# Performance work log

Measured on AMD Instinct MI355X. Metric: run time of the kernel, lower is better.

Reference implementation:

```python
import jax, jax.numpy as jnp
import numpy as np

IN_F = 4096
OUT_F = 11008
BATCH = 4
SEQ = 2048


def setup_inputs() -> dict:
    key = jax.random.key(0)
    kx, kw, ks = jax.random.split(key, 3)
    x = jax.random.normal(kx, (BATCH, SEQ, IN_F), dtype=jnp.float32)
    # simulated int4 weights stored in an int container, range [0, 16)
    W_q = jax.random.randint(kw, (OUT_F, IN_F), 0, 16, dtype=jnp.int32)
    scale = jax.random.uniform(ks, (OUT_F,), dtype=jnp.float32)
    return {"x": x, "W_q": W_q, "scale": scale}


def reference(x, W_q, scale):
    # dequantize: per-output-channel scale, then y = x @ W_fp^T
    W_fp = W_q.astype(jnp.float32) * scale[:, None]  # [out, in]
    return jnp.einsum('bsi,oi->bso', x, W_fp)
```

## Files before the change

kernel.cpp:

```cpp
#include <hip/hip_runtime.h>
#include <math.h>

#define M_DIM 8192
#define N_DIM 11008
#define K_DIM 4096

#define BM 256
#define BN 128
#define BKB 128
#define NT (K_DIM / BKB)
#define NBN (N_DIM / BN)
#define NWG ((M_DIM / BM) * NBN)

#define B_OFF 32768

typedef int int4v __attribute__((ext_vector_type(4)));
typedef int int16v __attribute__((ext_vector_type(16)));

__device__ __forceinline__ void async_copy16(const void* g, void* l) {
  __builtin_amdgcn_global_load_lds(
      (const __attribute__((address_space(1))) void*)g,
      (__attribute__((address_space(3))) void*)l, 16, 0, 0);
}

__global__ __launch_bounds__(256) void quant_x(const float* __restrict__ x,
                                               signed char* __restrict__ xq,
                                               float* __restrict__ sx) {
  __shared__ float wred[4];
  const int row = blockIdx.x;
  const int tid = threadIdx.x;
  const float4* src = (const float4*)(x + (size_t)row * K_DIM) + tid * 4;
  float4 v0 = src[0], v1 = src[1], v2 = src[2], v3 = src[3];

  float m = 0.f;
#define MX4(V) m = fmaxf(m, fmaxf(fmaxf(fabsf(V.x), fabsf(V.y)), fmaxf(fabsf(V.z), fabsf(V.w))))
  MX4(v0); MX4(v1); MX4(v2); MX4(v3);
#undef MX4
#pragma unroll
  for (int off = 32; off >= 1; off >>= 1)
    m = fmaxf(m, __shfl_xor(m, off, 64));
  if ((tid & 63) == 0) wred[tid >> 6] = m;
  __syncthreads();
  float smax = fmaxf(fmaxf(wred[0], wred[1]), fmaxf(wred[2], wred[3]));
  smax = fmaxf(smax, 1e-20f);
  const float inv = 127.f / smax;

  int4v o;
#define Q4(V, G) o[G] = ((int)rintf(V.x * inv) & 255) | (((int)rintf(V.y * inv) & 255) << 8) | \
                        (((int)rintf(V.z * inv) & 255) << 16) | (((int)rintf(V.w * inv) & 255) << 24)
  Q4(v0, 0); Q4(v1, 1); Q4(v2, 2); Q4(v3, 3);
#undef Q4
  ((int4v*)(xq + (size_t)row * K_DIM))[tid] = o;
  if (tid == 0) sx[row] = smax / 127.f;
}

__global__ __launch_bounds__(256) void pack_w(const int* __restrict__ in,
                                              signed char* __restrict__ wq) {
  const int idx = blockIdx.x * 256 + threadIdx.x;
  const int4* in4 = (const int4*)in + (size_t)idx * 4;
  int4 a = in4[0], b = in4[1], c = in4[2], d = in4[3];
  int4v o;
  o[0] = a.x | (a.y << 8) | (a.z << 16) | (a.w << 24);
  o[1] = b.x | (b.y << 8) | (b.z << 16) | (b.w << 24);
  o[2] = c.x | (c.y << 8) | (c.z << 16) | (c.w << 24);
  o[3] = d.x | (d.y << 8) | (d.z << 16) | (d.w << 24);
  ((int4v*)wq)[idx] = o;
}

__device__ __forceinline__ void stage_g(const signed char* __restrict__ P,
                                        int grow0, int k0b, char* dest, int tid) {
  const int r = tid >> 3;
  const int key = (r & 7) ^ ((tid >> 7) & 1);
  const int c = (tid & 7) ^ key;
  async_copy16(&P[(size_t)(grow0 + r) * K_DIM + k0b + c * 16], dest + tid * 16);
}

__global__ __launch_bounds__(512, 2) void gemm_i8(
    const signed char* __restrict__ A, const signed char* __restrict__ B,
    const float* __restrict__ scale, const float* __restrict__ sx,
    float* __restrict__ out) {
  __shared__ __align__(16) char smw[49152];
  const int tid = threadIdx.x;
  const int lane = tid & 63;
  const int wv = tid >> 6;
  const int wr = wv >> 1, wc = wv & 1;
  const int l31 = lane & 31;
  const int h = lane >> 5;
  const int swz = (l31 & 7) ^ ((l31 >> 4) & 1);

  int id = blockIdx.x;
  id = (id & 7) * (NWG / 8) + (id >> 3);
  const int bn = (id % NBN) * BN;
  const int bm = (id / NBN) * BM;

  int16v acc[2][2] = {};

#pragma unroll 1
  for (int t = 0; t < NT; ++t) {
    const int kb = t * BKB;
    __builtin_amdgcn_s_barrier();
    stage_g(A, bm,       kb, smw,         tid);
    stage_g(A, bm + 64,  kb, smw +  8192, tid);
    stage_g(A, bm + 128, kb, smw + 16384, tid);
    stage_g(A, bm + 192, kb, smw + 24576, tid);
    stage_g(B, bn,       kb, smw + B_OFF,        tid);
    stage_g(B, bn + 64,  kb, smw + B_OFF + 8192, tid);
    asm volatile("s_waitcnt vmcnt(0)" ::: "memory");
    __builtin_amdgcn_s_barrier();

#pragma unroll
    for (int ks = 0; ks < 4; ++ks) {
      const int cb = ((2 * ks + h) ^ swz) * 16;
      int4v af[2], bfr[2];
#pragma unroll
      for (int mi = 0; mi < 2; ++mi)
        af[mi] = *(const int4v*)(smw + (wr * 64 + mi * 32 + l31) * 128 + cb);
#pragma unroll
      for (int ni = 0; ni < 2; ++ni)
        bfr[ni] = *(const int4v*)(smw + B_OFF + (wc * 64 + ni * 32 + l31) * 128 + cb);
      __builtin_amdgcn_s_setprio(1);
#pragma unroll
      for (int mi = 0; mi < 2; ++mi)
#pragma unroll
        for (int ni = 0; ni < 2; ++ni)
          acc[mi][ni] = __builtin_amdgcn_mfma_i32_32x32x32_i8(
              af[mi], bfr[ni], acc[mi][ni], 0, 0, 0);
      __builtin_amdgcn_s_setprio(0);
    }
  }

  const int ocol0 = bn + wc * 64 + l31;
  const int orow0 = bm + wr * 64 + 4 * h;
#pragma unroll
  for (int ni = 0; ni < 2; ++ni) {
    const float sc = scale[ocol0 + ni * 32];
#pragma unroll
    for (int mi = 0; mi < 2; ++mi) {
#pragma unroll
      for (int reg = 0; reg < 16; ++reg) {
        const int row = orow0 + mi * 32 + (reg & 3) + 8 * (reg >> 2);
        out[(size_t)row * N_DIM + ocol0 + ni * 32] =
            (float)acc[mi][ni][reg] * sx[row] * sc;
      }
    }
  }
}

__global__ __launch_bounds__(256) void gemm_fallback(
    const float* __restrict__ X, const int* __restrict__ Wq,
    const float* __restrict__ scale, float* __restrict__ out) {
  __shared__ float Xs[64][17];
  __shared__ float Ws[64][17];
  const int tid = threadIdx.x;
  const int tn = blockIdx.x % (N_DIM / 64);
  const int tm = blockIdx.x / (N_DIM / 64);
  const int tr = tid >> 4, tc = tid & 15;
  float acc[4][4] = {};
  for (int k0 = 0; k0 < K_DIM; k0 += 16) {
#pragma unroll
    for (int i = 0; i < 4; ++i) {
      int idx = tid + i * 256;
      int r = idx >> 4, c = idx & 15;
      Xs[r][c] = X[(size_t)(tm * 64 + r) * K_DIM + k0 + c];
      Ws[r][c] = (float)Wq[(size_t)(tn * 64 + r) * K_DIM + k0 + c];
    }
    __syncthreads();
#pragma unroll
    for (int kk = 0; kk < 16; ++kk)
#pragma unroll
      for (int i = 0; i < 4; ++i) {
        float a = Xs[tr * 4 + i][kk];
#pragma unroll
        for (int j = 0; j < 4; ++j) acc[i][j] += a * Ws[tc * 4 + j][kk];
      }
    __syncthreads();
  }
#pragma unroll
  for (int i = 0; i < 4; ++i)
#pragma unroll
    for (int j = 0; j < 4; ++j) {
      int row = tm * 64 + tr * 4 + i, col = tn * 64 + tc * 4 + j;
      out[(size_t)row * N_DIM + col] = acc[i][j] * scale[col];
    }
}

extern "C" void kernel_launch(void* const* d_in, const int* in_sizes, int n_in,
                              void* d_out, int out_size, void* d_ws, size_t ws_size,
                              hipStream_t stream) {
  const float* x = (const float*)d_in[0];
  const int* Wq = (const int*)d_in[1];
  const float* scale = (const float*)d_in[2];
  float* out = (float*)d_out;

  const size_t XN = (size_t)M_DIM * K_DIM;
  const size_t WN = (size_t)N_DIM * K_DIM;
  const size_t need = XN + WN + M_DIM * sizeof(float);

  if (ws_size >= need) {
    signed char* xq = (signed char*)d_ws;
    signed char* wq = xq + XN;
    float* sx = (float*)(wq + WN);
    quant_x<<<M_DIM, 256, 0, stream>>>(x, xq, sx);
    pack_w<<<(unsigned)(WN / 4096), 256, 0, stream>>>(Wq, wq);
    gemm_i8<<<NWG, 512, 0, stream>>>(xq, wq, scale, sx, out);
  } else {
    gemm_fallback<<<(N_DIM / 64) * (M_DIM / 64), 256, 0, stream>>>(x, Wq, scale, out);
  }
}
```

Before: 494.0 us.

## Use chunk-transposed int8 layouts, load A to registers, double-buffer B in LDS

Both quantization kernels now write their int8 outputs in a K-chunk-major layout, with each 16-byte K chunk stored contiguously across rows or columns. The GEMM no longer stages A in shared memory: each wave loads its A fragments straight from global memory into registers, one K step ahead. Only B is staged in LDS, using a small double buffer with the K step halved. The smaller LDS footprint allows a higher occupancy hint. In exchange, A fragments shared by the two column waves are fetched twice from global/L1, and the transposed writes in quant_x become strided.

```diff
diff --git a/kernel.cpp b/kernel.cpp
--- a/kernel.cpp
+++ b/kernel.cpp
@@ -7,12 +7,13 @@
 
 #define BM 256
 #define BN 128
-#define BKB 128
+#define BKB 64
 #define NT (K_DIM / BKB)
 #define NBN (N_DIM / BN)
 #define NWG ((M_DIM / BM) * NBN)
 
-#define B_OFF 32768
+#define CHUNK_A_STRIDE (M_DIM * 16)
+#define CHUNK_B_STRIDE (N_DIM * 16)
 
 typedef int int4v __attribute__((ext_vector_type(4)));
 typedef int int16v __attribute__((ext_vector_type(16)));
@@ -24,7 +25,7 @@
 }
 
 __global__ __launch_bounds__(256) void quant_x(const float* __restrict__ x,
-                                               signed char* __restrict__ xq,
+                                               signed char* __restrict__ xqt,
                                                float* __restrict__ sx) {
   __shared__ float wred[4];
   const int row = blockIdx.x;
@@ -50,43 +51,36 @@
                         (((int)rintf(V.z * inv) & 255) << 16) | (((int)rintf(V.w * inv) & 255) << 24)
   Q4(v0, 0); Q4(v1, 1); Q4(v2, 2); Q4(v3, 3);
 #undef Q4
-  ((int4v*)(xq + (size_t)row * K_DIM))[tid] = o;
+  ((int4v*)xqt)[(size_t)tid * M_DIM + row] = o;
   if (tid == 0) sx[row] = smax / 127.f;
 }
 
 __global__ __launch_bounds__(256) void pack_w(const int* __restrict__ in,
-                                              signed char* __restrict__ wq) {
-  const int idx = blockIdx.x * 256 + threadIdx.x;
-  const int4* in4 = (const int4*)in + (size_t)idx * 4;
-  int4 a = in4[0], b = in4[1], c = in4[2], d = in4[3];
+                                              signed char* __restrict__ wqt) {
+  const int cg = blockIdx.x % (N_DIM / 256);
+  const int c = blockIdx.x / (N_DIM / 256);
+  const int col = cg * 256 + threadIdx.x;
+  const int4* src = (const int4*)(in + (size_t)col * K_DIM + c * 16);
+  int4 a = src[0], b = src[1], d = src[2], e = src[3];
   int4v o;
   o[0] = a.x | (a.y << 8) | (a.z << 16) | (a.w << 24);
   o[1] = b.x | (b.y << 8) | (b.z << 16) | (b.w << 24);
-  o[2] = c.x | (c.y << 8) | (c.z << 16) | (c.w << 24);
-  o[3] = d.x | (d.y << 8) | (d.z << 16) | (d.w << 24);
-  ((int4v*)wq)[idx] = o;
-}
-
-__device__ __forceinline__ void stage_g(const signed char* __restrict__ P,
-                                        int grow0, int k0b, char* dest, int tid) {
-  const int r = tid >> 3;
-  const int key = (r & 7) ^ ((tid >> 7) & 1);
-  const int c = (tid & 7) ^ key;
-  async_copy16(&P[(size_t)(grow0 + r) * K_DIM + k0b + c * 16], dest + tid * 16);
-}
-
-__global__ __launch_bounds__(512, 2) void gemm_i8(
+  o[2] = d.x | (d.y << 8) | (d.z << 16) | (d.w << 24);
+  o[3] = e.x | (e.y << 8) | (e.z << 16) | (e.w << 24);
+  ((int4v*)wqt)[(size_t)c * N_DIM + col] = o;
+}
+
+__global__ __launch_bounds__(512, 4) void gemm_i8(
     const signed char* __restrict__ A, const signed char* __restrict__ B,
     const float* __restrict__ scale, const float* __restrict__ sx,
     float* __restrict__ out) {
-  __shared__ __align__(16) char smw[49152];
+  __shared__ __align__(16) char smw[16384];
   const int tid = threadIdx.x;
   const int lane = tid & 63;
   const int wv = tid >> 6;
   const int wr = wv >> 1, wc = wv & 1;
   const int l31 = lane & 31;
   const int h = lane >> 5;
-  const int swz = (l31 & 7) ^ ((l31 >> 4) & 1);
 
   int id = blockIdx.x;
   id = (id & 7) * (NWG / 8) + (id >> 3);
@@ -95,37 +89,57 @@
 
   int16v acc[2][2] = {};
 
+  const signed char* Abase =
+      A + (size_t)h * CHUNK_A_STRIDE + (size_t)(bm + wr * 64 + l31) * 16;
+  const signed char* Bsrc0 =
+      B + (size_t)(tid >> 7) * CHUNK_B_STRIDE + (size_t)(bn + (tid & 127)) * 16;
+
+#define STAGE_B(T, OFF) \
+  async_copy16(Bsrc0 + (size_t)(4 * (T)) * CHUNK_B_STRIDE, smw + (OFF) + tid * 16)
+
+#define LOAD_A(T, SET)                                                        \
+  _Pragma("unroll") for (int ks = 0; ks < 2; ++ks)                            \
+  _Pragma("unroll") for (int mi = 0; mi < 2; ++mi)                            \
+    SET[ks][mi] = *(const int4v*)(Abase +                                     \
+        (size_t)(4 * (T) + 2 * ks) * CHUNK_A_STRIDE + mi * 32 * 16);
+
+#define COMPUTE(SET, OFF)                                                     \
+  _Pragma("unroll") for (int ks = 0; ks < 2; ++ks) {                          \
+    int4v bfr[2];                                                             \
+    _Pragma("unroll") for (int ni = 0; ni < 2; ++ni)                          \
+      bfr[ni] = *(const int4v*)(smw + (OFF) + (2 * ks + h) * 2048 +           \
+                                (wc * 64 + ni * 32 + l31) * 16);              \
+    __builtin_amdgcn_s_setprio(1);                                            \
+    _Pragma("unroll") for (int mi = 0; mi < 2; ++mi)                          \
+    _Pragma("unroll") for (int ni = 0; ni < 2; ++ni)                          \
+      acc[mi][ni] = __builtin_amdgcn_mfma_i32_32x32x32_i8(                    \
+          SET[ks][mi], bfr[ni], acc[mi][ni], 0, 0, 0);                        \
+    __builtin_amdgcn_s_setprio(0);                                            \
+  }
+
+  int4v AX[2][2], AY[2][2];
+
+  STAGE_B(0, 0);
+  LOAD_A(0, AX);
+  asm volatile("s_waitcnt vmcnt(0)" ::: "memory");
+  __builtin_amdgcn_s_barrier();
+
 #pragma unroll 1
-  for (int t = 0; t < NT; ++t) {
-    const int kb = t * BKB;
-    __builtin_amdgcn_s_barrier();
-    stage_g(A, bm,       kb, smw,         tid);
-    stage_g(A, bm + 64,  kb, smw +  8192, tid);
-    stage_g(A, bm + 128, kb, smw + 16384, tid);
-    stage_g(A, bm + 192, kb, smw + 24576, tid);
-    stage_g(B, bn,       kb, smw + B_OFF,        tid);
-    stage_g(B, bn + 64,  kb, smw + B_OFF + 8192, tid);
+  for (int t = 0; t < NT; t += 2) {
+    STAGE_B(t + 1, 8192);
+    LOAD_A(t + 1, AY);
+    COMPUTE(AX, 0);
     asm volatile("s_waitcnt vmcnt(0)" ::: "memory");
     __builtin_amdgcn_s_barrier();
 
-#pragma unroll
-    for (int ks = 0; ks < 4; ++ks) {
-      const int cb = ((2 * ks + h) ^ swz) * 16;
-      int4v af[2], bfr[2];
-#pragma unroll
-      for (int mi = 0; mi < 2; ++mi)
-        af[mi] = *(const int4v*)(smw + (wr * 64 + mi * 32 + l31) * 128 + cb);
-#pragma unroll
-      for (int ni = 0; ni < 2; ++ni)
-        bfr[ni] = *(const int4v*)(smw + B_OFF + (wc * 64 + ni * 32 + l31) * 128 + cb);
-      __builtin_amdgcn_s_setprio(1);
-#pragma unroll
-      for (int mi = 0; mi < 2; ++mi)
-#pragma unroll
-        for (int ni = 0; ni < 2; ++ni)
-          acc[mi][ni] = __builtin_amdgcn_mfma_i32_32x32x32_i8(
-              af[mi], bfr[ni], acc[mi][ni], 0, 0, 0);
-      __builtin_amdgcn_s_setprio(0);
+    if (t + 2 < NT) {
+      STAGE_B(t + 2, 0);
+      LOAD_A(t + 2, AX);
+    }
+    COMPUTE(AY, 8192);
+    if (t + 2 < NT) {
+      asm volatile("s_waitcnt vmcnt(0)" ::: "memory");
+      __builtin_amdgcn_s_barrier();
     }
   }
 
@@ -144,6 +158,9 @@
       }
     }
   }
+#undef STAGE_B
+#undef LOAD_A
+#undef COMPUTE
 }
 
 __global__ __launch_bounds__(256) void gemm_fallback(
@@ -197,12 +214,12 @@
   const size_t need = XN + WN + M_DIM * sizeof(float);
 
   if (ws_size >= need) {
-    signed char* xq = (signed char*)d_ws;
-    signed char* wq = xq + XN;
-    float* sx = (float*)(wq + WN);
-    quant_x<<<M_DIM, 256, 0, stream>>>(x, xq, sx);
-    pack_w<<<(unsigned)(WN / 4096), 256, 0, stream>>>(Wq, wq);
-    gemm_i8<<<NWG, 512, 0, stream>>>(xq, wq, scale, sx, out);
+    signed char* xqt = (signed char*)d_ws;
+    signed char* wqt = xqt + XN;
+    float* sx = (float*)(wqt + WN);
+    quant_x<<<M_DIM, 256, 0, stream>>>(x, xqt, sx);
+    pack_w<<<(N_DIM / 256) * 256, 256, 0, stream>>>(Wq, wqt);
+    gemm_i8<<<NWG, 512, 0, stream>>>(xqt, wqt, scale, sx, out);
   } else {
     gemm_fallback<<<(N_DIM / 64) * (M_DIM / 64), 256, 0, stream>>>(x, Wq, scale, out);
   }
```

After: 513.1 us. 3.9% more time.

## Enlarge int8 GEMM tile to 256x256 with double-buffered LDS prefetch pipeline

Applied to the files above, without the earlier changes.

Widens the output tile from 256x128 to 256x256 so each of the 8 waves computes a 128x64 sub-tile, which raises MFMA work per byte loaded from LDS and from global memory. The K loop now uses a double-buffered 128 KB LDS region. Global-to-LDS async copies for the next K step are issued in quarter chunks between four phases of MFMA work, so load latency overlaps compute instead of sitting behind a full wait and barrier. In exchange, occupancy drops to one workgroup per CU, register pressure rises with 8 accumulators, and the hand-placed waitcnt and barrier scheme must be exactly right to avoid races.

```diff
diff --git a/kernel.cpp b/kernel.cpp
--- a/kernel.cpp
+++ b/kernel.cpp
@@ -6,13 +6,11 @@
 #define K_DIM 4096
 
 #define BM 256
-#define BN 128
+#define BN 256
 #define BKB 128
 #define NT (K_DIM / BKB)
 #define NBN (N_DIM / BN)
 #define NWG ((M_DIM / BM) * NBN)
-
-#define B_OFF 32768
 
 typedef int int4v __attribute__((ext_vector_type(4)));
 typedef int int16v __attribute__((ext_vector_type(16)));
@@ -67,75 +65,168 @@
   ((int4v*)wq)[idx] = o;
 }
 
-__device__ __forceinline__ void stage_g(const signed char* __restrict__ P,
-                                        int grow0, int k0b, char* dest, int tid) {
-  const int r = tid >> 3;
-  const int key = (r & 7) ^ ((tid >> 7) & 1);
+__device__ __forceinline__ void stage_h(const signed char* __restrict__ P,
+                                        int grow0, int kbyte, char* dest, int tid) {
+  const int rl = tid >> 3;
+  const int key = (rl & 7) ^ ((rl >> 4) & 1);
   const int c = (tid & 7) ^ key;
-  async_copy16(&P[(size_t)(grow0 + r) * K_DIM + k0b + c * 16], dest + tid * 16);
-}
-
-__global__ __launch_bounds__(512, 2) void gemm_i8(
+  async_copy16(&P[(size_t)(grow0 + rl) * K_DIM + kbyte + c * 16], dest + tid * 16);
+}
+
+__global__ __launch_bounds__(512, 1) void gemm_i8(
     const signed char* __restrict__ A, const signed char* __restrict__ B,
     const float* __restrict__ scale, const float* __restrict__ sx,
     float* __restrict__ out) {
-  __shared__ __align__(16) char smw[49152];
+  __shared__ __align__(16) char smw[131072];
   const int tid = threadIdx.x;
   const int lane = tid & 63;
   const int wv = tid >> 6;
-  const int wr = wv >> 1, wc = wv & 1;
+  const int wr = wv >> 2, wc = wv & 3;
   const int l31 = lane & 31;
   const int h = lane >> 5;
-  const int swz = (l31 & 7) ^ ((l31 >> 4) & 1);
+  const int keyL = (l31 & 7) ^ ((l31 >> 4) & 1);
 
   int id = blockIdx.x;
   id = (id & 7) * (NWG / 8) + (id >> 3);
   const int bn = (id % NBN) * BN;
   const int bm = (id / NBN) * BM;
 
-  int16v acc[2][2] = {};
+  int16v acc[4][2] = {};
+
+#define RD_A(DST, BASE, KS, MIA)                                              \
+  DST = *(const int4v*)((BASE) + (wr * 2 + ((MIA) >> 1)) * 8192 +             \
+                        (((MIA) & 1) * 32 + l31) * 128 +                      \
+                        (((2 * (KS) + h) ^ keyL) << 4));
+#define RD_B(DST, BASE, KS, NN)                                               \
+  DST = *(const int4v*)((BASE) + 32768 + wc * 8192 +                          \
+                        ((NN) * 32 + l31) * 128 +                             \
+                        (((2 * (KS) + h) ^ keyL) << 4));
+
+  stage_h(B, bn,       0, smw + 32768, tid);
+  stage_h(B, bn +  64, 0, smw + 40960, tid);
+  stage_h(B, bn + 128, 0, smw + 49152, tid);
+  stage_h(B, bn + 192, 0, smw + 57344, tid);
+  stage_h(A, bm,       0, smw,         tid);
+  stage_h(A, bm + 128, 0, smw + 16384, tid);
+  stage_h(A, bm +  64, 0, smw +  8192, tid);
+  stage_h(A, bm + 192, 0, smw + 24576, tid);
+  asm volatile("s_waitcnt vmcnt(2)" ::: "memory");
+  __builtin_amdgcn_s_barrier();
+
+  int4v aA[2][2], aB[2][2], bL[2][2], bH[2][2];
 
 #pragma unroll 1
   for (int t = 0; t < NT; ++t) {
-    const int kb = t * BKB;
-    __builtin_amdgcn_s_barrier();
-    stage_g(A, bm,       kb, smw,         tid);
-    stage_g(A, bm + 64,  kb, smw +  8192, tid);
-    stage_g(A, bm + 128, kb, smw + 16384, tid);
-    stage_g(A, bm + 192, kb, smw + 24576, tid);
-    stage_g(B, bn,       kb, smw + B_OFF,        tid);
-    stage_g(B, bn + 64,  kb, smw + B_OFF + 8192, tid);
-    asm volatile("s_waitcnt vmcnt(0)" ::: "memory");
-    __builtin_amdgcn_s_barrier();
-
-#pragma unroll
-    for (int ks = 0; ks < 4; ++ks) {
-      const int cb = ((2 * ks + h) ^ swz) * 16;
-      int4v af[2], bfr[2];
-#pragma unroll
-      for (int mi = 0; mi < 2; ++mi)
-        af[mi] = *(const int4v*)(smw + (wr * 64 + mi * 32 + l31) * 128 + cb);
-#pragma unroll
-      for (int ni = 0; ni < 2; ++ni)
-        bfr[ni] = *(const int4v*)(smw + B_OFF + (wc * 64 + ni * 32 + l31) * 128 + cb);
-      __builtin_amdgcn_s_setprio(1);
-#pragma unroll
-      for (int mi = 0; mi < 2; ++mi)
-#pragma unroll
-        for (int ni = 0; ni < 2; ++ni)
-          acc[mi][ni] = __builtin_amdgcn_mfma_i32_32x32x32_i8(
-              af[mi], bfr[ni], acc[mi][ni], 0, 0, 0);
-      __builtin_amdgcn_s_setprio(0);
+    const char* cb = smw + (t & 1) * 65536;
+    char* nb = smw + ((t + 1) & 1) * 65536;
+    const int k1 = (t + 1) * BKB;
+    const bool pf = (t + 1 < NT);
+
+#pragma unroll
+    for (int s = 0; s < 2; ++s)
+#pragma unroll
+      for (int i = 0; i < 2; ++i) { RD_A(aA[s][i], cb, s, i); }
+#pragma unroll
+    for (int s = 0; s < 2; ++s)
+#pragma unroll
+      for (int n = 0; n < 2; ++n) { RD_B(bL[s][n], cb, s, n); }
+    if (pf) { stage_h(B, bn, k1, nb + 32768, tid);
+              stage_h(B, bn + 64, k1, nb + 40960, tid); }
+    __builtin_amdgcn_s_barrier();
+    asm volatile("s_waitcnt lgkmcnt(0)" ::: "memory");
+    __builtin_amdgcn_sched_barrier(0);
+    __builtin_amdgcn_s_setprio(1);
+#pragma unroll
+    for (int s = 0; s < 2; ++s)
+#pragma unroll
+      for (int i = 0; i < 2; ++i)
+#pragma unroll
+        for (int n = 0; n < 2; ++n)
+          acc[i][n] = __builtin_amdgcn_mfma_i32_32x32x32_i8(
+              aA[s][i], bL[s][n], acc[i][n], 0, 0, 0);
+    __builtin_amdgcn_s_setprio(0);
+    if (pf) asm volatile("s_waitcnt vmcnt(2)" ::: "memory");
+    else    asm volatile("s_waitcnt vmcnt(0)" ::: "memory");
+    __builtin_amdgcn_s_barrier();
+
+#pragma unroll
+    for (int s = 0; s < 2; ++s)
+#pragma unroll
+      for (int i = 0; i < 2; ++i) { RD_A(aB[s][i], cb, s, i + 2); }
+    if (pf) { stage_h(B, bn + 128, k1, nb + 49152, tid);
+              stage_h(B, bn + 192, k1, nb + 57344, tid); }
+    __builtin_amdgcn_s_barrier();
+    asm volatile("s_waitcnt lgkmcnt(0)" ::: "memory");
+    __builtin_amdgcn_sched_barrier(0);
+    __builtin_amdgcn_s_setprio(1);
+#pragma unroll
+    for (int s = 0; s < 2; ++s)
+#pragma unroll
+      for (int i = 0; i < 2; ++i)
+#pragma unroll
+        for (int n = 0; n < 2; ++n)
+          acc[i + 2][n] = __builtin_amdgcn_mfma_i32_32x32x32_i8(
+              aB[s][i], bL[s][n], acc[i + 2][n], 0, 0, 0);
+    __builtin_amdgcn_s_setprio(0);
+    __builtin_amdgcn_s_barrier();
+
+#pragma unroll
+    for (int s = 0; s < 2; ++s)
+#pragma unroll
+      for (int i = 0; i < 2; ++i) { RD_A(aA[s][i], cb, s + 2, i); }
+#pragma unroll
+    for (int s = 0; s < 2; ++s)
+#pragma unroll
+      for (int n = 0; n < 2; ++n) { RD_B(bH[s][n], cb, s + 2, n); }
+    if (pf) { stage_h(A, bm, k1, nb, tid);
+              stage_h(A, bm + 128, k1, nb + 16384, tid); }
+    __builtin_amdgcn_s_barrier();
+    asm volatile("s_waitcnt lgkmcnt(0)" ::: "memory");
+    __builtin_amdgcn_sched_barrier(0);
+    __builtin_amdgcn_s_setprio(1);
+#pragma unroll
+    for (int s = 0; s < 2; ++s)
+#pragma unroll
+      for (int i = 0; i < 2; ++i)
+#pragma unroll
+        for (int n = 0; n < 2; ++n)
+          acc[i][n] = __builtin_amdgcn_mfma_i32_32x32x32_i8(
+              aA[s][i], bH[s][n], acc[i][n], 0, 0, 0);
+    __builtin_amdgcn_s_setprio(0);
+    __builtin_amdgcn_s_barrier();
+
+#pragma unroll
+    for (int s = 0; s < 2; ++s)
+#pragma unroll
+      for (int i = 0; i < 2; ++i) { RD_A(aB[s][i], cb, s + 2, i + 2); }
+    if (pf) { stage_h(A, bm + 64, k1, nb + 8192, tid);
+              stage_h(A, bm + 192, k1, nb + 24576, tid); }
+    __builtin_amdgcn_s_barrier();
+    asm volatile("s_waitcnt lgkmcnt(0)" ::: "memory");
+    __builtin_amdgcn_sched_barrier(0);
+    __builtin_amdgcn_s_setprio(1);
+#pragma unroll
+    for (int s = 0; s < 2; ++s)
+#pragma unroll
+      for (int i = 0; i < 2; ++i)
+#pragma unroll
+        for (int n = 0; n < 2; ++n)
+          acc[i + 2][n] = __builtin_amdgcn_mfma_i32_32x32x32_i8(
+              aB[s][i], bH[s][n], acc[i + 2][n], 0, 0, 0);
+    __builtin_amdgcn_s_setprio(0);
+    if (pf) {
+      asm volatile("s_waitcnt vmcnt(2)" ::: "memory");
+      __builtin_amdgcn_s_barrier();
     }
   }
 
   const int ocol0 = bn + wc * 64 + l31;
-  const int orow0 = bm + wr * 64 + 4 * h;
+  const int orow0 = bm + wr * 128 + 4 * h;
 #pragma unroll
   for (int ni = 0; ni < 2; ++ni) {
     const float sc = scale[ocol0 + ni * 32];
 #pragma unroll
-    for (int mi = 0; mi < 2; ++mi) {
+    for (int mi = 0; mi < 4; ++mi) {
 #pragma unroll
       for (int reg = 0; reg < 16; ++reg) {
         const int row = orow0 + mi * 32 + (reg & 3) + 8 * (reg >> 2);
@@ -144,6 +235,8 @@
       }
     }
   }
+#undef RD_A
+#undef RD_B
 }
 
 __global__ __launch_bounds__(256) void gemm_fallback(
```

Measured after the change: 477.5 us (median of 2 runs). -3.3%, faster.
